# Optimization experiments

Hardware: AMD Instinct MI355X
Metric: run time of the kernel (lower is better)

The kernel has to match this reference:

```python
import jax, jax.numpy as jnp
import numpy as np
from jax import lax

B, C, H, W = 16, 128, 192, 192
KEY_POINTS = 512


def setup_inputs() -> dict:
    key = jax.random.key(0)
    ks = jax.random.split(key, 7)
    features = jax.random.normal(ks[0], (B, C, H, W), dtype=jnp.float32)
    # SimpleAttention: Conv2d(C, C, 1) -> weight [C, C], bias [C]
    attn_w = jax.random.normal(ks[1], (C, C), dtype=jnp.float32) * (1.0 / np.sqrt(C))
    attn_b = jnp.zeros((C,), dtype=jnp.float32)
    # Conv2d(C, 64, 3, padding=1)
    conv1_w = jax.random.normal(ks[2], (64, C, 3, 3), dtype=jnp.float32) * (1.0 / np.sqrt(C * 9))
    conv1_b = jnp.zeros((64,), dtype=jnp.float32)
    # Conv2d(64, 2, 1)
    conv2_w = jax.random.normal(ks[3], (2, 64), dtype=jnp.float32) * (1.0 / np.sqrt(64))
    conv2_b = jnp.zeros((2,), dtype=jnp.float32)
    return {
        "features": features,
        "attn_w": attn_w,
        "attn_b": attn_b,
        "conv1_w": conv1_w,
        "conv1_b": conv1_b,
        "conv2_w": conv2_w,
        "conv2_b": conv2_b,
    }


def _forward(features, attn_w, attn_b, conv1_w, conv1_b, conv2_w, conv2_b):
    b, c, h, w = features.shape
    # SimpleAttention: global avg pool -> 1x1 conv -> sigmoid -> scale
    pool = jnp.mean(features, axis=(2, 3))                       # [B, C]
    attn = jax.nn.sigmoid(pool @ attn_w.T + attn_b)               # [B, C]
    x = features * attn[:, :, None, None]                        # [B, C, H, W]
    # Conv2d(C, 64, 3, padding=1) + GELU (exact, torch default)
    y = lax.conv_general_dilated(
        x, conv1_w, window_strides=(1, 1), padding=((1, 1), (1, 1)),
        dimension_numbers=("NCHW", "OIHW", "NCHW"))
    y = jax.nn.gelu(y + conv1_b[None, :, None, None], approximate=False)
    # Conv2d(64, 2, 1)
    sparse_output = jnp.einsum("bchw,oc->bohw", y, conv2_w) + conv2_b[None, :, None, None]
    depth_pred = sparse_output[:, 0:1]                            # [B, 1, H, W]
    confidence = sparse_output[:, 1:2]                            # [B, 1, H, W]
    # softmax over flattened spatial dims
    confidence = jax.nn.softmax(confidence.reshape(b, -1), axis=1).reshape(b, 1, h, w)
    # avg_pool2d(k=3, s=1, p=1) with count_include_pad=True (torch default): divide by 9
    confidence = lax.reduce_window(
        confidence, 0.0, lax.add, (1, 1, 3, 3), (1, 1, 1, 1),
        ((0, 0), (0, 0), (1, 1), (1, 1))) / 9.0
    conf_flat = confidence.reshape(b, -1)                         # [B, H*W]
    depth_flat = depth_pred.reshape(b, -1)                        # [B, H*W]
    k = min(KEY_POINTS, h * w)
    _, indices = lax.top_k(conf_flat, k)                          # [B, k]
    sparse_depths = jnp.take_along_axis(depth_flat, indices, axis=1)  # [B, k]
    y_idx = (indices // w).astype(jnp.float32) / h
    x_idx = (indices % w).astype(jnp.float32) / w
    sparse_points = jnp.stack([x_idx, y_idx, sparse_depths], axis=2)  # [B, k, 3]
    return sparse_points, depth_pred, confidence


def reference(features, attn_w, attn_b, conv1_w, conv1_b, conv2_w, conv2_b):
    return _forward(features, attn_w, attn_b, conv1_w, conv1_b, conv2_w, conv2_b)
```

## Files before the change

### kernel.cpp

```cpp
#include <hip/hip_runtime.h>
#include <math.h>

#define BATCH 16
#define CIN   128
#define HH    192
#define WW    192
#define HW    (HH*WW)
#define OC    64
#define KPTS  512
#define CAP   2048
#define UMAX  (CAP*9)
#define LBLK  768
#define PPB   8

typedef short short8 __attribute__((ext_vector_type(8)));
typedef float f32x4 __attribute__((ext_vector_type(4)));

__device__ __forceinline__ unsigned short rne_bf16(float v) {
  unsigned u = __float_as_uint(v);
  u += 0x7FFFu + ((u >> 16) & 1u);
  return (unsigned short)(u >> 16);
}

__global__ __launch_bounds__(256) void pool_kernel(const float* __restrict__ feat,
                                                   double* __restrict__ pool) {
  int bc = blockIdx.x;
  const float4* fp = (const float4*)(feat + (size_t)bc * HW);
  double s = 0.0;
  for (int i = threadIdx.x; i < HW/4; i += 256) {
    float4 v = fp[i];
    s += (double)v.x + (double)v.y + (double)v.z + (double)v.w;
  }
  for (int off = 32; off > 0; off >>= 1) s += __shfl_down(s, off, 64);
  __shared__ double sb[4];
  int lane = threadIdx.x & 63, wv = threadIdx.x >> 6;
  if (lane == 0) sb[wv] = s;
  __syncthreads();
  if (threadIdx.x == 0) {
    double t = sb[0] + sb[1] + sb[2] + sb[3];
    pool[bc] = t / 36864.0;
  }
}

__global__ __launch_bounds__(128) void attn_kernel(const double* __restrict__ pool,
                                                   const float* __restrict__ attn_w,
                                                   const float* __restrict__ attn_b,
                                                   double* __restrict__ attn_d,
                                                   float* __restrict__ attn_f) {
  __shared__ double sp[CIN];
  int b = blockIdx.x, c = threadIdx.x;
  sp[c] = pool[b*CIN + c];
  __syncthreads();
  double s = (double)attn_b[c];
  const float* wr = attn_w + (size_t)c * CIN;
  for (int j = 0; j < CIN; j++) s = fma((double)wr[j], sp[j], s);
  double a = 1.0 / (1.0 + exp(-s));
  attn_d[b*CIN + c] = a;
  attn_f[b*CIN + c] = (float)a;
}

__global__ __launch_bounds__(256) void wtrans_kernel(const float* __restrict__ w,
                                                     unsigned short* __restrict__ wb_h,
                                                     unsigned short* __restrict__ wb_l) {
  int i = blockIdx.x * 256 + threadIdx.x;
  if (i < OC*CIN*9) {
    int oc = i / (CIN*9);
    int r  = i % (CIN*9);
    int c  = r / 9;
    int k  = r % 9;
    float v = w[i];
    unsigned short h = rne_bf16(v);
    float hf = __uint_as_float((unsigned)h << 16);
    wb_h[((size_t)k*OC + oc)*CIN + c] = h;
    wb_l[((size_t)k*OC + oc)*CIN + c] = rne_bf16(v - hf);
  }
}

__global__ __launch_bounds__(256) void wscale64_kernel(const float* __restrict__ w,
                                                       const double* __restrict__ attn_d,
                                                       double* __restrict__ wab64p) {
  const int b = blockIdx.y;
  int i = blockIdx.x * 256 + threadIdx.x;
  if (i < CIN*OC*10) {
    int kk = i % 10;
    int co = i / 10;
    int oc = co & 63, c = co >> 6;
    double v = 0.0;
    if (kk < 9) v = (double)w[((size_t)oc*CIN + c)*9 + kk] * attn_d[b*CIN + c];
    wab64p[(((size_t)b*CIN + c)*OC + oc)*10 + kk] = v;
  }
}

__global__ __launch_bounds__(256) void xpose_kernel(const float* __restrict__ feat,
                                                    const float* __restrict__ attn_f,
                                                    unsigned short* __restrict__ xp_h,
                                                    unsigned short* __restrict__ xp_l,
                                                    float* __restrict__ xq,
                                                    int b0) {
  __shared__ float lds[64*130];
  __shared__ float s_attn[CIN];
  const int bl = blockIdx.y;
  const int b  = b0 + bl;
  const int px0 = blockIdx.x * 64;
  const int tid = threadIdx.x;
  const int lane = tid & 63, wq = tid >> 6;

  if (tid < CIN) s_attn[tid] = attn_f[b*CIN + tid];
  #pragma unroll 8
  for (int k = 0; k < 32; k++) {
    int c = wq + 4*k;
    lds[lane*130 + c] = feat[((size_t)(b*CIN + c))*HW + px0 + lane];
  }
  __syncthreads();

  const int px = tid >> 2, cq = tid & 3;
  size_t base = ((size_t)bl*HW + px0 + px)*CIN + cq*32;
  float4* xqp = (float4*)(xq + base);
  #pragma unroll
  for (int half = 0; half < 4; half++) {
    short8 hv, lv;
    float4 q0, q1;
    #pragma unroll
    for (int j = 0; j < 8; j++) {
      int c = cq*32 + half*8 + j;
      float raw = lds[px*130 + c];
      float v = raw * s_attn[c];
      unsigned short h = rne_bf16(v);
      hv[j] = (short)h;
      lv[j] = (short)rne_bf16(v - __uint_as_float((unsigned)h << 16));
      if (j < 4) ((float*)&q0)[j] = raw; else ((float*)&q1)[j-4] = raw;
    }
    *reinterpret_cast<short8*>(xp_h + base + half*8) = hv;
    *reinterpret_cast<short8*>(xp_l + base + half*8) = lv;
    xqp[half*2]     = q0;
    xqp[half*2 + 1] = q1;
  }
}

#define TLH 18
#define TLW 18
#define CST 36
__global__ __launch_bounds__(256, 3) void conv_kernel(const unsigned short* __restrict__ xp_h,
                                                      const unsigned short* __restrict__ xp_l,
                                                      const unsigned short* __restrict__ wb_h,
                                                      const unsigned short* __restrict__ wb_l,
                                                      const float* __restrict__ conv1_b,
                                                      const float* __restrict__ conv2_w,
                                                      const float* __restrict__ conv2_b,
                                                      float* __restrict__ depth_out,
                                                      float* __restrict__ logit_out,
                                                      int b0, int nwg) {
  int bid = blockIdx.x;
  int q = nwg >> 3, r = nwg & 7;
  int xcd = bid & 7, pos = bid >> 3;
  int swz = (xcd < r ? xcd*(q+1) : r*(q+1) + (xcd - r)*q) + pos;
  const int bl = swz / 144;
  const int t144 = swz % 144;
  const int b  = b0 + bl;
  const int h0 = (t144 / 12) * 16, w0 = (t144 % 12) * 16;
  const int tid = threadIdx.x;
  const int wv = tid >> 6, ln = tid & 63;
  const int lg = ln >> 4, lr = ln & 15;

  __shared__ __align__(16) unsigned short th[TLH*TLW*CST];
  __shared__ __align__(16) unsigned short tl[TLH*TLW*CST];

  f32x4 acc[4][4];
  #pragma unroll
  for (int mi = 0; mi < 4; mi++)
    #pragma unroll
    for (int ni = 0; ni < 4; ni++)
      acc[mi][ni] = (f32x4){0.f, 0.f, 0.f, 0.f};

  const short8 zero8 = (short8){0,0,0,0,0,0,0,0};

  #pragma unroll 1
  for (int c0 = 0; c0 < CIN; c0 += 32) {
    __syncthreads();
    for (int u = tid; u < 2*TLH*TLW*4; u += 256) {
      int pl = u / (TLH*TLW*4);
      int rest = u - pl*(TLH*TLW*4);
      int rr  = rest / (TLW*4);
      int rw  = rest - rr*(TLW*4);
      int col = rw >> 2, sub = rw & 3;
      int gh = h0 + rr - 1, gw = w0 + col - 1;
      short8 val = zero8;
      if (gh >= 0 && gh < HH && gw >= 0 && gw < WW) {
        const unsigned short* src = (pl ? xp_l : xp_h)
            + ((size_t)(bl*HH + gh)*WW + gw)*CIN + c0 + sub*8;
        val = *reinterpret_cast<const short8*>(src);
      }
      unsigned short* dst = (pl ? tl : th) + ((rr*TLW + col)*CST + sub*8);
      *reinterpret_cast<short8*>(dst) = val;
    }
    __syncthreads();

    #pragma unroll
    for (int v = 0; v < 3; v++) {
      short8 ah[6], al[6];
      #pragma unroll
      for (int r6 = 0; r6 < 6; r6++) {
        int off = ((4*wv + r6)*TLW + lr + v)*CST + 8*lg;
        ah[r6] = *reinterpret_cast<const short8*>(&th[off]);
        al[r6] = *reinterpret_cast<const short8*>(&tl[off]);
      }
      #pragma unroll
      for (int u = 0; u < 3; u++) {
        short8 bh[4], blo[4];
        #pragma unroll
        for (int ni = 0; ni < 4; ni++) {
          size_t woff = ((size_t)(u*3 + v)*OC + ni*16 + lr)*CIN + c0 + 8*lg;
          bh[ni]  = *reinterpret_cast<const short8*>(wb_h + woff);
          blo[ni] = *reinterpret_cast<const short8*>(wb_l + woff);
        }
        #pragma unroll
        for (int mi = 0; mi < 4; mi++) {
          #pragma unroll
          for (int ni = 0; ni < 4; ni++) {
            acc[mi][ni] = __builtin_amdgcn_mfma_f32_16x16x32_bf16(ah[mi+u], bh[ni],  acc[mi][ni], 0, 0, 0);
            acc[mi][ni] = __builtin_amdgcn_mfma_f32_16x16x32_bf16(ah[mi+u], blo[ni], acc[mi][ni], 0, 0, 0);
            acc[mi][ni] = __builtin_amdgcn_mfma_f32_16x16x32_bf16(al[mi+u], bh[ni],  acc[mi][ni], 0, 0, 0);
          }
        }
      }
    }
  }

  float bia[4], w20[4], w21[4];
  #pragma unroll
  for (int ni = 0; ni < 4; ni++) {
    int oc = ni*16 + lr;
    bia[ni] = conv1_b[oc];
    w20[ni] = conv2_w[oc];
    w21[ni] = conv2_w[OC + oc];
  }
  const float c2b0 = conv2_b[0], c2b1 = conv2_b[1];

  #pragma unroll
  for (int mi = 0; mi < 4; mi++) {
    const int gh = h0 + 4*wv + mi;
    #pragma unroll
    for (int q2 = 0; q2 < 4; q2++) {
      float s0 = 0.f, s1 = 0.f;
      #pragma unroll
      for (int ni = 0; ni < 4; ni++) {
        float z = acc[mi][ni][q2] + bia[ni];
        float g = 0.5f * z * (1.0f + erff(z * 0.70710678118654752f));
        s0 = fmaf(g, w20[ni], s0);
        s1 = fmaf(g, w21[ni], s1);
      }
      #pragma unroll
      for (int m = 1; m <= 8; m <<= 1) {
        s0 += __shfl_xor(s0, m, 64);
        s1 += __shfl_xor(s1, m, 64);
      }
      if (lr == 0) {
        const int gw = w0 + 4*lg + q2;
        depth_out[((size_t)b*HH + gh)*WW + gw] = s0 + c2b0;
        logit_out[((size_t)b*HH + gh)*WW + gw] = s1 + c2b1;
      }
    }
  }
}

__global__ __launch_bounds__(1024) void softmax_kernel(float* __restrict__ logits,
                                                       float* __restrict__ m_out,
                                                       int b0) {
  const int b = b0 + blockIdx.x;
  float* lp = logits + (size_t)b * HW;
  const int tid = threadIdx.x;
  __shared__ float sred[16];
  __shared__ float s_m, s_z;

  float m = -INFINITY;
  for (int i = tid; i < HW; i += 1024) m = fmaxf(m, lp[i]);
  for (int off = 32; off > 0; off >>= 1) m = fmaxf(m, __shfl_down(m, off, 64));
  if ((tid & 63) == 0) sred[tid >> 6] = m;
  __syncthreads();
  if (tid == 0) {
    float t = sred[0];
    for (int i = 1; i < 16; i++) t = fmaxf(t, sred[i]);
    s_m = t;
    m_out[b] = t;
  }
  __syncthreads();
  m = s_m;

  float z = 0.f;
  for (int i = tid; i < HW; i += 1024) z += expf(lp[i] - m);
  __syncthreads();
  for (int off = 32; off > 0; off >>= 1) z += __shfl_down(z, off, 64);
  if ((tid & 63) == 0) sred[tid >> 6] = z;
  __syncthreads();
  if (tid == 0) {
    float t = 0.f;
    for (int i = 0; i < 16; i++) t += sred[i];
    s_z = t;
  }
  __syncthreads();
  z = s_z;

  for (int i = tid; i < HW; i += 1024) lp[i] = expf(lp[i] - m) / z;
}

__global__ __launch_bounds__(256) void box_kernel(const float* __restrict__ p,
                                                  float* __restrict__ out_f,
                                                  int b0, int g) {
  int i = blockIdx.x * 256 + threadIdx.x;
  if (i >= g * HW) return;
  int b = b0 + i / HW, r = i % HW, h = r / WW, w = r % WW;
  const float* bp = p + (size_t)b * HW;
  float s = 0.f;
  for (int dy = -1; dy <= 1; dy++) {
    int h2 = h + dy;
    if (h2 < 0 || h2 >= HH) continue;
    for (int dx = -1; dx <= 1; dx++) {
      int w2 = w + dx;
      if (w2 < 0 || w2 >= WW) continue;
      s += bp[h2*WW + w2];
    }
  }
  out_f[(size_t)b*HW + r] = s / 9.0f;
}

__global__ __launch_bounds__(1024) void cand_kernel(const float* __restrict__ conf,
                                                    int* __restrict__ cand_idx,
                                                    int* __restrict__ cand_cnt,
                                                    int* __restrict__ upix,
                                                    int* __restrict__ upix_cnt,
                                                    int b0) {
  const int b = b0 + blockIdx.x;
  const float* cp = conf + (size_t)b * HW;
  const int tid = threadIdx.x;
  __shared__ unsigned sred[16];
  __shared__ unsigned s_total;
  __shared__ unsigned s_cnt;
  __shared__ unsigned bm[1152];
  __shared__ unsigned pcs[1152];
  __shared__ unsigned grpoff[37];

  unsigned lo = 0u, hi = 0x7F800000u;
  while (hi - lo > 1u) {
    unsigned mid = lo + ((hi - lo) >> 1);
    unsigned cnt = 0;
    for (int i = tid; i < HW; i += 1024)
      cnt += (__float_as_uint(cp[i]) >= mid) ? 1u : 0u;
    for (int off = 32; off > 0; off >>= 1) cnt += __shfl_down(cnt, off, 64);
    if ((tid & 63) == 0) sred[tid >> 6] = cnt;
    __syncthreads();
    if (tid == 0) {
      unsigned t = 0;
      for (int i = 0; i < 16; i++) t += sred[i];
      s_total = t;
    }
    __syncthreads();
    unsigned total = s_total;
    __syncthreads();
    if (total >= KPTS) lo = mid; else hi = mid;
  }
  float vcut = __uint_as_float(lo) * (1.0f - 1e-4f);

  if (tid == 0) s_cnt = 0;
  for (int i = tid; i < 1152; i += 1024) bm[i] = 0u;
  __syncthreads();

  for (int i = tid; i < HW; i += 1024) {
    if (cp[i] >= vcut) {
      unsigned s = atomicAdd(&s_cnt, 1u);
      if (s < CAP) {
        cand_idx[b*CAP + s] = i;
        int h = i / WW, w = i % WW;
        for (int dy = -1; dy <= 1; dy++) {
          int qh = h + dy;
          if (qh < 0 || qh >= HH) continue;
          for (int dx = -1; dx <= 1; dx++) {
            int qw = w + dx;
            if (qw < 0 || qw >= WW) continue;
            int q = qh*WW + qw;
            atomicOr(&bm[q >> 5], 1u << (q & 31));
          }
        }
      }
    }
  }
  __syncthreads();
  if (tid == 0) cand_cnt[b] = (s_cnt < CAP) ? s_cnt : CAP;

  for (int i = tid; i < 1152; i += 1024) pcs[i] = __popc(bm[i]);
  __syncthreads();
  if (tid < 36) {
    unsigned s = 0;
    for (int j = 0; j < 32; j++) s += pcs[tid*32 + j];
    grpoff[tid] = s;
  }
  __syncthreads();
  if (tid == 0) {
    unsigned run = 0;
    for (int g2 = 0; g2 < 36; g2++) { unsigned t = grpoff[g2]; grpoff[g2] = run; run += t; }
    grpoff[36] = run;
    upix_cnt[b] = (int)run;
  }
  __syncthreads();
  for (int i = tid; i < 1152; i += 1024) {
    unsigned off = grpoff[i >> 5];
    for (int w = (i & ~31); w < i; w++) off += pcs[w];
    unsigned u = bm[i];
    while (u) {
      int bit = __ffs(u) - 1;
      u &= u - 1u;
      upix[b*UMAX + off++] = i*32 + bit;
    }
  }
}

__global__ __launch_bounds__(256) void logit_kernel(const float* __restrict__ xq,
                                                    const double* __restrict__ wab64p,
                                                    const float* __restrict__ conv1_b,
                                                    const float* __restrict__ conv2_w,
                                                    const float* __restrict__ conv2_b,
                                                    const int* __restrict__ upix,
                                                    const int* __restrict__ upix_cnt,
                                                    double* __restrict__ lmap,
                                                    int b0, int nb) {
  int bid = blockIdx.x;
  int swz = (bid & 7) * (nb >> 3) + (bid >> 3);
  const int bl = swz / LBLK;
  const int b  = b0 + bl;
  const int slot0 = swz % LBLK;
  const int ucnt = upix_cnt[b];
  const int tid = threadIdx.x;

  __shared__ __align__(16) float xf[PPB][1536];
  __shared__ double part[4][PPB][64];
  __shared__ int    s_pix[PPB];

  for (int base = slot0*PPB; base < ucnt; base += LBLK*PPB) {
    const int rem = min(PPB, ucnt - base);
    if (tid < PPB) s_pix[tid] = (tid < rem) ? upix[b*UMAX + base + tid] : 0;
    __syncthreads();

    for (int i = tid; i < PPB*9*32; i += 256) {
      int p = i / 288;
      int r = i % 288;
      int k = r >> 5, t = r & 31;
      float4 v = (float4){0.f, 0.f, 0.f, 0.f};
      if (p < rem) {
        int pix = s_pix[p];
        int gh = pix / WW + k/3 - 1, gw = pix % WW + k%3 - 1;
        if (gh >= 0 && gh < HH && gw >= 0 && gw < WW)
          v = *reinterpret_cast<const float4*>(
                xq + ((size_t)(bl*HW + gh*WW + gw))*CIN + 4*t);
      }
      int cb = 4*t;
      xf[p][(cb+0)*12 + k] = v.x;
      xf[p][(cb+1)*12 + k] = v.y;
      xf[p][(cb+2)*12 + k] = v.z;
      xf[p][(cb+3)*12 + k] = v.w;
    }
    __syncthreads();

    const int oc = tid & 63, cq = tid >> 6;
    double acc[PPB];
    #pragma unroll
    for (int p = 0; p < PPB; p++) acc[p] = 0.0;
    const double* wp = wab64p + (((size_t)b*CIN + cq*32)*OC + oc)*10;
    for (int cc = 0; cc < 32; cc++) {
      const int c = cq*32 + cc;
      double2 wv[5];
      #pragma unroll
      for (int q = 0; q < 5; q++) wv[q] = *((const double2*)wp + q);
      wp += OC*10;
      #pragma unroll
      for (int p = 0; p < PPB; p++) {
        const float4* xp = (const float4*)&xf[p][c*12];
        float4 a = xp[0], bb = xp[1], cc4 = xp[2];
        double t = acc[p];
        t = fma(wv[0].x, (double)a.x,  t);
        t = fma(wv[0].y, (double)a.y,  t);
        t = fma(wv[1].x, (double)a.z,  t);
        t = fma(wv[1].y, (double)a.w,  t);
        t = fma(wv[2].x, (double)bb.x, t);
        t = fma(wv[2].y, (double)bb.y, t);
        t = fma(wv[3].x, (double)bb.z, t);
        t = fma(wv[3].y, (double)bb.w, t);
        t = fma(wv[4].x, (double)cc4.x, t);
        acc[p] = t;
      }
    }
    #pragma unroll
    for (int p = 0; p < PPB; p++) part[cq][p][oc] = acc[p];
    __syncthreads();

    for (int t0 = tid; t0 < PPB*64; t0 += 256) {
      const int p = t0 >> 6, o = t0 & 63;
      double z = part[0][p][o] + part[1][p][o] + part[2][p][o] + part[3][p][o]
               + (double)conv1_b[o];
      double g = 0.5 * z * (1.0 + erf(z * 0.70710678118654752440));
      double cv = g * (double)conv2_w[OC + o];
      #pragma unroll
      for (int m = 1; m <= 32; m <<= 1) cv += __shfl_xor(cv, m, 64);
      if (o == 0 && p < rem)
        lmap[(size_t)b*HW + s_pix[p]] = cv + (double)conv2_b[1];
    }
    __syncthreads();
  }
}

__global__ __launch_bounds__(256) void score_kernel(const double* __restrict__ lmap,
                                                    const float* __restrict__ m32,
                                                    const int* __restrict__ cand_idx,
                                                    const int* __restrict__ cand_cnt,
                                                    double* __restrict__ cand_score,
                                                    int b0) {
  const int b = b0 + blockIdx.y;
  const int slot = blockIdx.x * 256 + threadIdx.x;
  if (slot >= cand_cnt[b]) return;
  const int idx = cand_idx[b*CAP + slot];
  const int ph = idx / WW, pw = idx % WW;
  const double m = (double)m32[b];
  double s = 0.0;
  for (int dy = -1; dy <= 1; dy++) {
    int qh = ph + dy;
    if (qh < 0 || qh >= HH) continue;
    for (int dx = -1; dx <= 1; dx++) {
      int qw = pw + dx;
      if (qw < 0 || qw >= WW) continue;
      s += exp(lmap[(size_t)b*HW + qh*WW + qw] - m);
    }
  }
  cand_score[b*CAP + slot] = s;
}

__global__ __launch_bounds__(1024) void emit_kernel(const double* __restrict__ cand_score,
                                                    const int* __restrict__ cand_idx,
                                                    const int* __restrict__ cand_cnt,
                                                    const float* __restrict__ depth,
                                                    float* __restrict__ points,
                                                    int b0) {
  const int b = b0 + blockIdx.x;
  const int tid = threadIdx.x;
  __shared__ double vals[CAP];
  __shared__ int    idxs[CAP];

  int cnt = cand_cnt[b];
  for (int i = tid; i < CAP; i += 1024) {
    if (i < cnt) { vals[i] = cand_score[b*CAP + i]; idxs[i] = cand_idx[b*CAP + i]; }
    else         { vals[i] = -1.0;                  idxs[i] = 0x7FFFFFFF; }
  }
  __syncthreads();

  for (unsigned k = 2; k <= CAP; k <<= 1) {
    for (unsigned j = k >> 1; j > 0; j >>= 1) {
      unsigned t = (unsigned)tid;
      unsigned i1 = ((t & ~(j - 1u)) << 1) | (t & (j - 1u));
      unsigned i2 = i1 | j;
      double v1 = vals[i1], v2 = vals[i2];
      int    a1 = idxs[i1], a2 = idxs[i2];
      bool oneAfterTwo = (v1 < v2) || (v1 == v2 && a1 > a2);
      bool descSeg = ((i1 & k) == 0);
      if (descSeg ? oneAfterTwo : !oneAfterTwo) {
        vals[i1] = v2; idxs[i1] = a2;
        vals[i2] = v1; idxs[i2] = a1;
      }
      __syncthreads();
    }
  }

  if (tid < KPTS) {
    int idx = idxs[tid];
    float d = depth[(size_t)b * HW + idx];
    float xi = (float)(idx % WW) / (float)WW;
    float yi = (float)(idx / WW) / (float)HH;
    float* pp = points + ((size_t)b * KPTS + tid) * 3;
    pp[0] = xi; pp[1] = yi; pp[2] = d;
  }
}

extern "C" void kernel_launch(void* const* d_in, const int* in_sizes, int n_in,
                              void* d_out, int out_size, void* d_ws, size_t ws_size,
                              hipStream_t stream) {
  const float* feat    = (const float*)d_in[0];
  const float* attn_w  = (const float*)d_in[1];
  const float* attn_b  = (const float*)d_in[2];
  const float* conv1_w = (const float*)d_in[3];
  const float* conv1_b = (const float*)d_in[4];
  const float* conv2_w = (const float*)d_in[5];
  const float* conv2_b = (const float*)d_in[6];

  float* out    = (float*)d_out;
  float* points = out;
  float* depth  = out + 24576;
  float* conf_f = out + 24576 + BATCH*HW;

  double* wsd        = (double*)d_ws;
  double* pool_d     = wsd;
  double* attn_d     = wsd + 2048;
  double* cand_score = wsd + 4096;
  double* lmap       = cand_score + BATCH*CAP;
  double* wab64p     = lmap + (size_t)BATCH*HW;
  float*  wsf        = (float*)(wab64p + (size_t)BATCH*CIN*OC*10);
  float*  logit32    = wsf;
  float*  attn_f     = logit32 + (size_t)BATCH*HW;
  float*  m32        = attn_f + 2048;
  unsigned short* wb_h = (unsigned short*)(m32 + 16);
  unsigned short* wb_l = wb_h + OC*CIN*9;
  int*    cand_idx   = (int*)(wb_l + OC*CIN*9);
  int*    cand_cnt   = cand_idx + BATCH*CAP;
  int*    upix       = cand_cnt + 16;
  int*    upix_cnt   = upix + BATCH*UMAX;
  size_t fixed_bytes = ((size_t)((char*)(upix_cnt + 16) - (char*)d_ws) + 255) & ~(size_t)255;
  char* dyn_base = (char*)d_ws + fixed_bytes;
  const size_t pbe = (size_t)HW * CIN;
  const size_t per_batch_bytes = 2*pbe*2 + pbe*4;
  size_t avail = (ws_size > fixed_bytes + 65536) ? (ws_size - fixed_bytes - 65536) : 0;
  int gb = (int)(avail / per_batch_bytes);
  if (gb > BATCH) gb = BATCH;
  if (gb < 1) gb = 1;
  unsigned short* xp_h = (unsigned short*)dyn_base;
  unsigned short* xp_l = xp_h + (size_t)gb * pbe;
  float*          xq   = (float*)(xp_l + (size_t)gb * pbe);

  pool_kernel<<<BATCH*CIN, 256, 0, stream>>>(feat, pool_d);
  attn_kernel<<<BATCH, CIN, 0, stream>>>(pool_d, attn_w, attn_b, attn_d, attn_f);
  wtrans_kernel<<<(OC*CIN*9 + 255)/256, 256, 0, stream>>>(conv1_w, wb_h, wb_l);
  wscale64_kernel<<<dim3((CIN*OC*10 + 255)/256, BATCH), 256, 0, stream>>>(conv1_w, attn_d, wab64p);

  for (int b0 = 0; b0 < BATCH; b0 += gb) {
    int g = (BATCH - b0 < gb) ? (BATCH - b0) : gb;
    xpose_kernel<<<dim3(HW/64, g), 256, 0, stream>>>(feat, attn_f, xp_h, xp_l, xq, b0);
    conv_kernel<<<g*144, 256, 0, stream>>>(xp_h, xp_l, wb_h, wb_l,
                                           conv1_b, conv2_w, conv2_b,
                                           depth, logit32, b0, g*144);
    softmax_kernel<<<g, 1024, 0, stream>>>(logit32, m32, b0);
    box_kernel<<<(g*HW + 255)/256, 256, 0, stream>>>(logit32, conf_f, b0, g);
    cand_kernel<<<g, 1024, 0, stream>>>(conf_f, cand_idx, cand_cnt, upix, upix_cnt, b0);
    logit_kernel<<<g*LBLK, 256, 0, stream>>>(xq, wab64p, conv1_b, conv2_w, conv2_b,
                                             upix, upix_cnt, lmap, b0, g*LBLK);
    score_kernel<<<dim3(CAP/256, g), 256, 0, stream>>>(lmap, m32, cand_idx, cand_cnt,
                                                       cand_score, b0);
    emit_kernel<<<g, 1024, 0, stream>>>(cand_score, cand_idx, cand_cnt, depth, points, b0);
  }
}
```

Baseline: 1.164 ms.

## Fuse pooling into transpose pass and split bf16 inside conv tile loads

Removes the separate full-read pooling kernel by computing per-channel partial sums inside the NHWC transpose kernel, followed by a small reduction kernel. The transpose now writes only the fp32 NHWC copy. The conv kernel reads that copy, applies the attention scale and does the hi/lo bf16 split while staging its LDS tile. This avoids one full pass over the input and the writes of two bf16 planes. In exchange the conv tile loads fetch twice the bytes (fp32) and do extra conversion ALU work, with halo pixels converted more than once.

```diff
diff --git a/kernel.cpp b/kernel.cpp
--- a/kernel.cpp
+++ b/kernel.cpp
@@ -12,6 +12,7 @@
 #define UMAX  (CAP*9)
 #define LBLK  768
 #define PPB   8
+#define NXB   (HW/64)
 
 typedef short short8 __attribute__((ext_vector_type(8)));
 typedef float f32x4 __attribute__((ext_vector_type(4)));
@@ -22,33 +23,65 @@
   return (unsigned short)(u >> 16);
 }
 
-__global__ __launch_bounds__(256) void pool_kernel(const float* __restrict__ feat,
-                                                   double* __restrict__ pool) {
-  int bc = blockIdx.x;
-  const float4* fp = (const float4*)(feat + (size_t)bc * HW);
+__global__ __launch_bounds__(256) void xq_kernel(const float* __restrict__ feat,
+                                                 float* __restrict__ xq,
+                                                 double* __restrict__ psum,
+                                                 int b0) {
+  __shared__ float lds[64*130];
+  const int bl = blockIdx.y;
+  const int b  = b0 + bl;
+  const int px0 = blockIdx.x * 64;
+  const int tid = threadIdx.x;
+  const int lane = tid & 63, wq = tid >> 6;
+
+  #pragma unroll 8
+  for (int k = 0; k < 32; k++) {
+    int c = wq + 4*k;
+    lds[lane*130 + c] = feat[((size_t)(b*CIN + c))*HW + px0 + lane];
+  }
+  __syncthreads();
+
+  if (tid < CIN) {
+    double s = 0.0;
+    #pragma unroll 8
+    for (int px = 0; px < 64; px++) s += (double)lds[px*130 + tid];
+    psum[((size_t)b*CIN + tid)*NXB + blockIdx.x] = s;
+  }
+
+  const int px = tid >> 2, cq = tid & 3;
+  size_t base = ((size_t)bl*HW + px0 + px)*CIN + cq*32;
+  float4* xqp = (float4*)(xq + base);
+  #pragma unroll
+  for (int half = 0; half < 8; half++) {
+    float4 q;
+    #pragma unroll
+    for (int j = 0; j < 4; j++)
+      ((float*)&q)[j] = lds[px*130 + cq*32 + half*4 + j];
+    xqp[half] = q;
+  }
+}
+
+__global__ __launch_bounds__(64) void poolreduce_kernel(const double* __restrict__ psum,
+                                                        double* __restrict__ pool,
+                                                        int b0) {
+  const int lb = blockIdx.x / CIN, c = blockIdx.x % CIN;
+  const int b = b0 + lb;
+  const int tid = threadIdx.x;
+  const double* pp = psum + ((size_t)b*CIN + c)*NXB;
   double s = 0.0;
-  for (int i = threadIdx.x; i < HW/4; i += 256) {
-    float4 v = fp[i];
-    s += (double)v.x + (double)v.y + (double)v.z + (double)v.w;
-  }
+  for (int j = tid; j < NXB; j += 64) s += pp[j];
   for (int off = 32; off > 0; off >>= 1) s += __shfl_down(s, off, 64);
-  __shared__ double sb[4];
-  int lane = threadIdx.x & 63, wv = threadIdx.x >> 6;
-  if (lane == 0) sb[wv] = s;
-  __syncthreads();
-  if (threadIdx.x == 0) {
-    double t = sb[0] + sb[1] + sb[2] + sb[3];
-    pool[bc] = t / 36864.0;
-  }
+  if (tid == 0) pool[b*CIN + c] = s / 36864.0;
 }
 
 __global__ __launch_bounds__(128) void attn_kernel(const double* __restrict__ pool,
                                                    const float* __restrict__ attn_w,
                                                    const float* __restrict__ attn_b,
                                                    double* __restrict__ attn_d,
-                                                   float* __restrict__ attn_f) {
+                                                   float* __restrict__ attn_f,
+                                                   int b0) {
   __shared__ double sp[CIN];
-  int b = blockIdx.x, c = threadIdx.x;
+  int b = b0 + blockIdx.x, c = threadIdx.x;
   sp[c] = pool[b*CIN + c];
   __syncthreads();
   double s = (double)attn_b[c];
@@ -78,8 +111,9 @@
 
 __global__ __launch_bounds__(256) void wscale64_kernel(const float* __restrict__ w,
                                                        const double* __restrict__ attn_d,
-                                                       double* __restrict__ wab64p) {
-  const int b = blockIdx.y;
+                                                       double* __restrict__ wab64p,
+                                                       int b0) {
+  const int b = b0 + blockIdx.y;
   int i = blockIdx.x * 256 + threadIdx.x;
   if (i < CIN*OC*10) {
     int kk = i % 10;
@@ -91,57 +125,11 @@
   }
 }
 
-__global__ __launch_bounds__(256) void xpose_kernel(const float* __restrict__ feat,
-                                                    const float* __restrict__ attn_f,
-                                                    unsigned short* __restrict__ xp_h,
-                                                    unsigned short* __restrict__ xp_l,
-                                                    float* __restrict__ xq,
-                                                    int b0) {
-  __shared__ float lds[64*130];
-  __shared__ float s_attn[CIN];
-  const int bl = blockIdx.y;
-  const int b  = b0 + bl;
-  const int px0 = blockIdx.x * 64;
-  const int tid = threadIdx.x;
-  const int lane = tid & 63, wq = tid >> 6;
-
-  if (tid < CIN) s_attn[tid] = attn_f[b*CIN + tid];
-  #pragma unroll 8
-  for (int k = 0; k < 32; k++) {
-    int c = wq + 4*k;
-    lds[lane*130 + c] = feat[((size_t)(b*CIN + c))*HW + px0 + lane];
-  }
-  __syncthreads();
-
-  const int px = tid >> 2, cq = tid & 3;
-  size_t base = ((size_t)bl*HW + px0 + px)*CIN + cq*32;
-  float4* xqp = (float4*)(xq + base);
-  #pragma unroll
-  for (int half = 0; half < 4; half++) {
-    short8 hv, lv;
-    float4 q0, q1;
-    #pragma unroll
-    for (int j = 0; j < 8; j++) {
-      int c = cq*32 + half*8 + j;
-      float raw = lds[px*130 + c];
-      float v = raw * s_attn[c];
-      unsigned short h = rne_bf16(v);
-      hv[j] = (short)h;
-      lv[j] = (short)rne_bf16(v - __uint_as_float((unsigned)h << 16));
-      if (j < 4) ((float*)&q0)[j] = raw; else ((float*)&q1)[j-4] = raw;
-    }
-    *reinterpret_cast<short8*>(xp_h + base + half*8) = hv;
-    *reinterpret_cast<short8*>(xp_l + base + half*8) = lv;
-    xqp[half*2]     = q0;
-    xqp[half*2 + 1] = q1;
-  }
-}
-
 #define TLH 18
 #define TLW 18
 #define CST 36
-__global__ __launch_bounds__(256, 3) void conv_kernel(const unsigned short* __restrict__ xp_h,
-                                                      const unsigned short* __restrict__ xp_l,
+__global__ __launch_bounds__(256, 3) void conv_kernel(const float* __restrict__ xq,
+                                                      const float* __restrict__ attn_f,
                                                       const unsigned short* __restrict__ wb_h,
                                                       const unsigned short* __restrict__ wb_l,
                                                       const float* __restrict__ conv1_b,
@@ -164,6 +152,9 @@
 
   __shared__ __align__(16) unsigned short th[TLH*TLW*CST];
   __shared__ __align__(16) unsigned short tl[TLH*TLW*CST];
+  __shared__ float s_attn[CIN];
+
+  if (tid < CIN) s_attn[tid] = attn_f[b*CIN + tid];
 
   f32x4 acc[4][4];
   #pragma unroll
@@ -177,21 +168,28 @@
   #pragma unroll 1
   for (int c0 = 0; c0 < CIN; c0 += 32) {
     __syncthreads();
-    for (int u = tid; u < 2*TLH*TLW*4; u += 256) {
-      int pl = u / (TLH*TLW*4);
-      int rest = u - pl*(TLH*TLW*4);
-      int rr  = rest / (TLW*4);
-      int rw  = rest - rr*(TLW*4);
+    for (int i = tid; i < TLH*TLW*4; i += 256) {
+      int rr  = i / (TLW*4);
+      int rw  = i % (TLW*4);
       int col = rw >> 2, sub = rw & 3;
       int gh = h0 + rr - 1, gw = w0 + col - 1;
-      short8 val = zero8;
+      short8 hv = zero8, lv = zero8;
       if (gh >= 0 && gh < HH && gw >= 0 && gw < WW) {
-        const unsigned short* src = (pl ? xp_l : xp_h)
-            + ((size_t)(bl*HH + gh)*WW + gw)*CIN + c0 + sub*8;
-        val = *reinterpret_cast<const short8*>(src);
-      }
-      unsigned short* dst = (pl ? tl : th) + ((rr*TLW + col)*CST + sub*8);
-      *reinterpret_cast<short8*>(dst) = val;
+        const float4* src = (const float4*)(xq
+            + ((size_t)(bl*HH + gh)*WW + gw)*CIN + c0 + sub*8);
+        float4 f0 = src[0], f1 = src[1];
+        #pragma unroll
+        for (int j = 0; j < 8; j++) {
+          float raw = (j < 4) ? ((const float*)&f0)[j] : ((const float*)&f1)[j-4];
+          float v = raw * s_attn[c0 + sub*8 + j];
+          unsigned short h = rne_bf16(v);
+          hv[j] = (short)h;
+          lv[j] = (short)rne_bf16(v - __uint_as_float((unsigned)h << 16));
+        }
+      }
+      int off = (rr*TLW + col)*CST + sub*8;
+      *reinterpret_cast<short8*>(&th[off]) = hv;
+      *reinterpret_cast<short8*>(&tl[off]) = lv;
     }
     __syncthreads();
 
@@ -598,7 +596,8 @@
   double* cand_score = wsd + 4096;
   double* lmap       = cand_score + BATCH*CAP;
   double* wab64p     = lmap + (size_t)BATCH*HW;
-  float*  wsf        = (float*)(wab64p + (size_t)BATCH*CIN*OC*10);
+  double* psum       = wab64p + (size_t)BATCH*CIN*OC*10;
+  float*  wsf        = (float*)(psum + (size_t)BATCH*CIN*NXB);
   float*  logit32    = wsf;
   float*  attn_f     = logit32 + (size_t)BATCH*HW;
   float*  m32        = attn_f + 2048;
@@ -611,24 +610,23 @@
   size_t fixed_bytes = ((size_t)((char*)(upix_cnt + 16) - (char*)d_ws) + 255) & ~(size_t)255;
   char* dyn_base = (char*)d_ws + fixed_bytes;
   const size_t pbe = (size_t)HW * CIN;
-  const size_t per_batch_bytes = 2*pbe*2 + pbe*4;
+  const size_t per_batch_bytes = pbe * 4;
   size_t avail = (ws_size > fixed_bytes + 65536) ? (ws_size - fixed_bytes - 65536) : 0;
   int gb = (int)(avail / per_batch_bytes);
   if (gb > BATCH) gb = BATCH;
   if (gb < 1) gb = 1;
-  unsigned short* xp_h = (unsigned short*)dyn_base;
-  unsigned short* xp_l = xp_h + (size_t)gb * pbe;
-  float*          xq   = (float*)(xp_l + (size_t)gb * pbe);
-
-  pool_kernel<<<BATCH*CIN, 256, 0, stream>>>(feat, pool_d);
-  attn_kernel<<<BATCH, CIN, 0, stream>>>(pool_d, attn_w, attn_b, attn_d, attn_f);
+  float* xq = (float*)dyn_base;
+
   wtrans_kernel<<<(OC*CIN*9 + 255)/256, 256, 0, stream>>>(conv1_w, wb_h, wb_l);
-  wscale64_kernel<<<dim3((CIN*OC*10 + 255)/256, BATCH), 256, 0, stream>>>(conv1_w, attn_d, wab64p);
 
   for (int b0 = 0; b0 < BATCH; b0 += gb) {
     int g = (BATCH - b0 < gb) ? (BATCH - b0) : gb;
-    xpose_kernel<<<dim3(HW/64, g), 256, 0, stream>>>(feat, attn_f, xp_h, xp_l, xq, b0);
-    conv_kernel<<<g*144, 256, 0, stream>>>(xp_h, xp_l, wb_h, wb_l,
+    xq_kernel<<<dim3(NXB, g), 256, 0, stream>>>(feat, xq, psum, b0);
+    poolreduce_kernel<<<g*CIN, 64, 0, stream>>>(psum, pool_d, b0);
+    attn_kernel<<<g, CIN, 0, stream>>>(pool_d, attn_w, attn_b, attn_d, attn_f, b0);
+    wscale64_kernel<<<dim3((CIN*OC*10 + 255)/256, g), 256, 0, stream>>>(conv1_w, attn_d,
+                                                                        wab64p, b0);
+    conv_kernel<<<g*144, 256, 0, stream>>>(xq, attn_f, wb_h, wb_l,
                                            conv1_b, conv2_w, conv2_b,
                                            depth, logit32, b0, g*144);
     softmax_kernel<<<g, 1024, 0, stream>>>(logit32, m32, b0);
```

Result: faster. 947.3 us (median of 3 runs) (-18.6%).
